# Optimization experiments

Measured on AMD Instinct MI355X. Metric: run time of the kernel, lower is better.

## Reference

```python
import jax, jax.numpy as jnp
import numpy as np
import math

EMBED_DIM = 256
NUM_HEADS = 8
FFN_DIM = 1024
EPS = 1e-5


def layer_norm(x, g, b):
    mu = jnp.mean(x, axis=-1, keepdims=True)
    var = jnp.var(x, axis=-1, keepdims=True)
    return (x - mu) / jnp.sqrt(var + EPS) * g + b


def setup_inputs() -> dict:
    key = jax.random.key(0)
    ks = jax.random.split(key, 10)
    B, L, D, F = 4, 2048, EMBED_DIM, FFN_DIM
    x = jax.random.normal(ks[0], (B, L, D), dtype=jnp.float32)
    mask = jnp.ones((B, L), dtype=jnp.int32)
    # FFN params (PyTorch Linear default-ish scale)
    W1 = jax.random.normal(ks[1], (D, F), dtype=jnp.float32) / np.sqrt(D)
    b1 = jnp.zeros((F,), dtype=jnp.float32)
    W2 = jax.random.normal(ks[2], (F, D), dtype=jnp.float32) / np.sqrt(F)
    b2 = jnp.zeros((D,), dtype=jnp.float32)
    g1 = jnp.ones((D,), dtype=jnp.float32)
    be1 = jnp.zeros((D,), dtype=jnp.float32)
    g2 = jnp.ones((D,), dtype=jnp.float32)
    be2 = jnp.zeros((D,), dtype=jnp.float32)
    return {"x": x, "mask": mask, "W1": W1, "b1": b1, "W2": W2, "b2": b2,
            "g1": g1, "be1": be1, "g2": g2, "be2": be2}


def quantum_attention(x, mask):
    B, L, D = x.shape
    H, dk = NUM_HEADS, D // NUM_HEADS
    xh = x.reshape(B, L, H, dk).transpose(0, 2, 1, 3)  # [B,H,L,dk]
    # per-token mean over batch and heads -> [L, dk]
    m = jnp.mean(xh, axis=(0, 1))
    # closed form of the single-qubit RX circuit: P(|1>) = sin^2(angle/2)
    dot = m @ m.T  # [L, L]
    ang = jnp.clip(dot, -math.pi, math.pi)
    scores = jnp.sin(ang * 0.5) ** 2  # [L, L], shared across B and H
    attn = jnp.broadcast_to(scores[None, None], (B, H, L, L))
    attn = jnp.where(mask[:, None, None, :] == 0, -1e9, attn)
    attn = jax.nn.softmax(attn, axis=-1)
    out = jnp.einsum('bhij,bhjd->bhid', attn, xh)  # values are xh itself
    return out.transpose(0, 2, 1, 3).reshape(B, L, D)


def reference(x, mask, W1, b1, W2, b2, g1, be1, g2, be2):
    attn_out = quantum_attention(x, mask)
    h = layer_norm(x + attn_out, g1, be1)
    ffn = jax.nn.relu(h @ W1 + b1) @ W2 + b2
    return layer_norm(h + ffn, g2, be2)
```

## Files before the change

kernel.cpp:

```cpp
#include <hip/hip_runtime.h>
#include <hip/hip_bf16.h>


#define B_ 4
#define L_ 2048
#define D_ 256
#define F_ 1024
#define PI_F 3.14159265358979323846f

typedef __bf16 bf16x8 __attribute__((ext_vector_type(8)));
typedef float floatx4 __attribute__((ext_vector_type(4)));

__device__ __forceinline__ unsigned short f2bf(float f) {
    unsigned int u = __float_as_uint(f);
    u = (u + 0x7FFFu + ((u >> 16) & 1u)) >> 16;
    return (unsigned short)u;
}
__device__ __forceinline__ float bf2f(unsigned short u) {
    union { unsigned int i; float f; } v; v.i = ((unsigned int)u) << 16; return v.f;
}

__device__ __forceinline__ void async_cp16(unsigned short* lds, const unsigned short* g) {
    __builtin_amdgcn_global_load_lds(
        (const __attribute__((address_space(1))) unsigned int*)g,
        (__attribute__((address_space(3))) unsigned int*)lds, 16, 0, 0);
}

__global__ __launch_bounds__(256) void k_prep(const float* __restrict__ x,
                                              const float* __restrict__ W1,
                                              const float* __restrict__ W2,
                                              const int* __restrict__ mask,
                                              unsigned short* __restrict__ mb,
                                              unsigned short* __restrict__ XmT,
                                              unsigned short* __restrict__ W1T,
                                              unsigned short* __restrict__ W2T) {
    __shared__ float tile[32][33];
    int r = blockIdx.x, t = threadIdx.x;
    if (r >= 2560) {
        if (r < 2816) {
            int idx = (r - 2560) * 256 + t;
            int l = idx >> 5, k = idx & 31;
            float s = 0.f;
#pragma unroll
            for (int b = 0; b < B_; b++) {
                const float* xp = x + ((size_t)(b * L_ + l)) * D_ + k;
#pragma unroll
                for (int h = 0; h < 8; h++) s += xp[h * 32];
            }
            mb[idx] = f2bf(s * (1.f / 32.f));
        } else {
#pragma unroll
            for (int c = 0; c < 32; c++) {
                int e = c * 256 + t;
                int b = e >> 11, j = e & (L_ - 1);
                XmT[(size_t)(1024 + b) * L_ + j] = mask[b * L_ + j] ? 0x3F80 : 0;
            }
        }
        return;
    }
    const float* in; unsigned short* outp; int R, C; const int* mrow = nullptr; size_t bo = 0;
    int bx, by;
    if (r < 2048) {
        int z = r >> 9, rem = r & 511; by = rem >> 3; bx = rem & 7;
        in = x; outp = XmT; R = L_; C = 256; bo = (size_t)z * R * C; mrow = mask + z * L_;
    } else if (r < 2304) {
        int rem = r - 2048; bx = rem & 31; by = rem >> 5;
        in = W1; outp = W1T; R = 256; C = 1024;
    } else {
        int rem = r - 2304; bx = rem & 7; by = rem >> 3;
        in = W2; outp = W2T; R = 1024; C = 256;
    }
    int r0 = by * 32, c0 = bx * 32;
    int tx = t & 31, ty = t >> 5;
#pragma unroll
    for (int rr = 0; rr < 4; rr++) {
        int rw = ty + rr * 8;
        tile[rw][tx] = in[bo + (size_t)(r0 + rw) * C + c0 + tx];
    }
    float mfac = 1.f;
    if (mrow) mfac = mrow[r0 + tx] ? 1.f : 0.f;
    __syncthreads();
#pragma unroll
    for (int rr = 0; rr < 4; rr++) {
        int c = ty + rr * 8;
        outp[bo + (size_t)(c0 + c) * R + r0 + tx] = f2bf(tile[tx][c] * mfac);
    }
}

__global__ __launch_bounds__(256) void k_scores_mfma(const unsigned short* __restrict__ mb,
                                                     unsigned short* __restrict__ E) {
    const int t = threadIdx.x, lane = t & 63, wid = t >> 6;
    const int wm = (wid >> 1) * 64, wn = (wid & 1) * 32;
    const int lr = lane & 15, lq = lane >> 4;
    int m0 = blockIdx.y * 128, n0 = blockIdx.x * 64;
    bf16x8 af[4], bfr[2];
#pragma unroll
    for (int i = 0; i < 4; i++)
        af[i] = *(const bf16x8*)(mb + (size_t)(m0 + wm + i * 16 + lr) * 32 + lq * 8);
#pragma unroll
    for (int j = 0; j < 2; j++)
        bfr[j] = *(const bf16x8*)(mb + (size_t)(n0 + wn + j * 16 + lr) * 32 + lq * 8);
    floatx4 acc[4][2];
#pragma unroll
    for (int i = 0; i < 4; i++)
#pragma unroll
        for (int j = 0; j < 2; j++) {
            acc[i][j] = (floatx4){0.f, 0.f, 0.f, 0.f};
            acc[i][j] = __builtin_amdgcn_mfma_f32_16x16x32_bf16(af[i], bfr[j], acc[i][j], 0, 0, 0);
        }
#pragma unroll
    for (int i = 0; i < 4; i++)
#pragma unroll
        for (int j = 0; j < 2; j++)
#pragma unroll
            for (int r = 0; r < 4; r++) {
                int row = m0 + wm + i * 16 + lq * 4 + r;
                int col = n0 + wn + j * 16 + lr;
                float d = fminf(fmaxf(acc[i][j][r], -PI_F), PI_F);
                float sn = __sinf(0.5f * d);
                E[(size_t)row * L_ + col] = f2bf(__expf(sn * sn));
            }
}

__device__ __forceinline__ void mfma_gemm_async(const unsigned short* __restrict__ A,
                                                const unsigned short* __restrict__ Bt,
                                                int K, int m0, int n0,
                                                unsigned short* sA, unsigned short* sB,
                                                floatx4 acc[4][2]) {
    const int t = threadIdx.x;
    const int lane = t & 63, wid = t >> 6;
    const int wm = (wid >> 1) * 64, wn = (wid & 1) * 32;
    const int lr = lane & 15, lq = lane >> 4;
    const int lrow = lane >> 3, lseg = lane & 7;

    const unsigned short* Ag[4]; unsigned short* sAd[4];
#pragma unroll
    for (int q = 0; q < 4; q++) {
        int rl = wid * 32 + q * 8 + lrow;
        int seg = (lseg - rl) & 7;
        Ag[q] = A + (size_t)(m0 + rl) * K + seg * 8;
        sAd[q] = sA + (wid * 32 + q * 8) * 64;
    }
    const unsigned short* Bg[2]; unsigned short* sBd[2];
#pragma unroll
    for (int q = 0; q < 2; q++) {
        int rl = wid * 16 + q * 8 + lrow;
        int seg = (lseg - rl) & 7;
        Bg[q] = Bt + (size_t)(n0 + rl) * K + seg * 8;
        sBd[q] = sB + (wid * 16 + q * 8) * 64;
    }
    int arot[4], brot[2];
    const unsigned short* sAr[4]; const unsigned short* sBr[2];
#pragma unroll
    for (int i = 0; i < 4; i++) { int ar = wm + i * 16 + lr; sAr[i] = sA + ar * 64; arot[i] = lq + ar; }
#pragma unroll
    for (int j = 0; j < 2; j++) { int br = wn + j * 16 + lr; sBr[j] = sB + br * 64; brot[j] = lq + br; }

    for (int k0 = 0; k0 < K; k0 += 64) {
        __syncthreads();
#pragma unroll
        for (int q = 0; q < 4; q++) async_cp16(sAd[q], Ag[q] + k0);
#pragma unroll
        for (int q = 0; q < 2; q++) async_cp16(sBd[q], Bg[q] + k0);
        __syncthreads();
#pragma unroll
        for (int s = 0; s < 2; s++) {
            bf16x8 af[4], bfr[2];
#pragma unroll
            for (int i = 0; i < 4; i++)
                af[i] = *(const bf16x8*)(sAr[i] + ((s * 4 + arot[i]) & 7) * 8);
#pragma unroll
            for (int j = 0; j < 2; j++)
                bfr[j] = *(const bf16x8*)(sBr[j] + ((s * 4 + brot[j]) & 7) * 8);
#pragma unroll
            for (int i = 0; i < 4; i++)
#pragma unroll
                for (int j = 0; j < 2; j++)
                    acc[i][j] = __builtin_amdgcn_mfma_f32_16x16x32_bf16(af[i], bfr[j], acc[i][j], 0, 0, 0);
        }
    }
}

__global__ __launch_bounds__(256) void k_av(const unsigned short* __restrict__ E,
                                            const unsigned short* __restrict__ XmT,
                                            unsigned short* __restrict__ Cb) {
    __shared__ __align__(16) unsigned short sA[128 * 64];
    __shared__ __align__(16) unsigned short sB[64 * 64];
    floatx4 acc[4][2];
#pragma unroll
    for (int i = 0; i < 4; i++)
#pragma unroll
        for (int j = 0; j < 2; j++) acc[i][j] = (floatx4){0.f, 0.f, 0.f, 0.f};
    int m0 = blockIdx.y * 128, n0 = blockIdx.x * 64;
    mfma_gemm_async(E, XmT, L_, m0, n0, sA, sB, acc);
    const int lane = threadIdx.x & 63, wid = threadIdx.x >> 6;
    const int wm = (wid >> 1) * 64, wn = (wid & 1) * 32;
    const int lr = lane & 15, lq = lane >> 4;
#pragma unroll
    for (int i = 0; i < 4; i++)
#pragma unroll
        for (int j = 0; j < 2; j++)
#pragma unroll
            for (int r = 0; r < 4; r++) {
                int row = m0 + wm + i * 16 + lq * 4 + r;
                int col = n0 + wn + j * 16 + lr;
                Cb[(size_t)row * 1088 + col] = f2bf(acc[i][j][r]);
            }
}

__global__ __launch_bounds__(256) void k_ln1(const float* __restrict__ x, const unsigned short* __restrict__ Cb,
                                             const float* __restrict__ g_, const float* __restrict__ be_,
                                             unsigned short* __restrict__ hb) {
    int tok = blockIdx.x, t = threadIdx.x;
    int b = tok >> 11, i = tok & (L_ - 1);
    float rs = bf2f(Cb[(size_t)i * 1088 + 1024 + b]);
    float v = x[(size_t)tok * D_ + t] + bf2f(Cb[(size_t)i * 1088 + b * 256 + t]) / rs;
    float s = v, s2 = v * v;
    __shared__ float sm[8];
#pragma unroll
    for (int o = 1; o < 64; o <<= 1) { s += __shfl_xor(s, o); s2 += __shfl_xor(s2, o); }
    if ((t & 63) == 0) { sm[t >> 6] = s; sm[4 + (t >> 6)] = s2; }
    __syncthreads();
    s = sm[0] + sm[1] + sm[2] + sm[3];
    s2 = sm[4] + sm[5] + sm[6] + sm[7];
    float mu = s * (1.f / 256.f);
    float var = s2 * (1.f / 256.f) - mu * mu;
    float r = rsqrtf(var + 1e-5f);
    hb[(size_t)tok * D_ + t] = f2bf((v - mu) * r * g_[t] + be_[t]);
}

__global__ __launch_bounds__(256) void k_gemm1(const unsigned short* __restrict__ hb,
                                               const unsigned short* __restrict__ W1T,
                                               const float* __restrict__ b1, unsigned short* __restrict__ t1) {
    __shared__ __align__(16) unsigned short sA[128 * 64];
    __shared__ __align__(16) unsigned short sB[128 * 64];
    const int t = threadIdx.x, lane = t & 63, wid = t >> 6;
    const int wm = (wid >> 1) * 64, wn = (wid & 1) * 64;
    const int lr = lane & 15, lq = lane >> 4;
    const int lrow8 = lane >> 3, lseg = lane & 7;
    int m0 = blockIdx.y * 128, n0 = blockIdx.x * 128;

    const unsigned short* Ag[4]; unsigned short* sAd[4];
    const unsigned short* Bg[4]; unsigned short* sBd[4];
#pragma unroll
    for (int q = 0; q < 4; q++) {
        int rl = q * 32 + wid * 8 + lrow8;
        int seg = (lseg - rl) & 7;
        Ag[q] = hb + (size_t)(m0 + rl) * 256 + seg * 8;
        Bg[q] = W1T + (size_t)(n0 + rl) * 256 + seg * 8;
        sAd[q] = sA + (q * 32 + wid * 8) * 64;
        sBd[q] = sB + (q * 32 + wid * 8) * 64;
    }
    const unsigned short* sAr[4]; int arot[4];
    const unsigned short* sBr[4]; int brot[4];
#pragma unroll
    for (int i = 0; i < 4; i++) { int ar = wm + i * 16 + lr; sAr[i] = sA + ar * 64; arot[i] = lq + ar; }
#pragma unroll
    for (int j = 0; j < 4; j++) { int br = wn + j * 16 + lr; sBr[j] = sB + br * 64; brot[j] = lq + br; }

    floatx4 acc[4][4];
#pragma unroll
    for (int i = 0; i < 4; i++)
#pragma unroll
        for (int j = 0; j < 4; j++) acc[i][j] = (floatx4){0.f, 0.f, 0.f, 0.f};

    for (int k0 = 0; k0 < 256; k0 += 64) {
        __syncthreads();
#pragma unroll
        for (int q = 0; q < 4; q++) { async_cp16(sAd[q], Ag[q] + k0); async_cp16(sBd[q], Bg[q] + k0); }
        __syncthreads();
#pragma unroll
        for (int s = 0; s < 2; s++) {
            bf16x8 af[4], bfr[4];
#pragma unroll
            for (int i = 0; i < 4; i++) af[i] = *(const bf16x8*)(sAr[i] + ((s * 4 + arot[i]) & 7) * 8);
#pragma unroll
            for (int j = 0; j < 4; j++) bfr[j] = *(const bf16x8*)(sBr[j] + ((s * 4 + brot[j]) & 7) * 8);
#pragma unroll
            for (int i = 0; i < 4; i++)
#pragma unroll
                for (int j = 0; j < 4; j++)
                    acc[i][j] = __builtin_amdgcn_mfma_f32_16x16x32_bf16(af[i], bfr[j], acc[i][j], 0, 0, 0);
        }
    }
    float bb[4];
#pragma unroll
    for (int j = 0; j < 4; j++) bb[j] = b1[n0 + wn + j * 16 + lr];
#pragma unroll
    for (int i = 0; i < 4; i++)
#pragma unroll
        for (int j = 0; j < 4; j++) {
            int col = n0 + wn + j * 16 + lr;
#pragma unroll
            for (int r = 0; r < 4; r++) {
                int row = m0 + wm + i * 16 + lq * 4 + r;
                t1[(size_t)row * 1024 + col] = f2bf(fmaxf(acc[i][j][r] + bb[j], 0.f));
            }
        }
}

__global__ __launch_bounds__(256) void k_gemm2ln(const unsigned short* __restrict__ t1,
                                                 const unsigned short* __restrict__ W2T,
                                                 const float* __restrict__ b2,
                                                 const unsigned short* __restrict__ hb,
                                                 const float* __restrict__ g_, const float* __restrict__ be_,
                                                 float* __restrict__ out) {
    __shared__ __align__(16) unsigned short sA[32 * 64];
    __shared__ __align__(16) unsigned short sB[256 * 64];
    __shared__ float red[2][32][2];
    const int t = threadIdx.x, lane = t & 63, wid = t >> 6;
    const int wm = (wid >> 1) * 16, wn = (wid & 1) * 128;
    const int lr = lane & 15, lq = lane >> 4;
    const int lrow8 = lane >> 3, lseg = lane & 7;
    int m0 = blockIdx.x * 32;

    int arl = wid * 8 + lrow8;
    const unsigned short* Ag = t1 + (size_t)(m0 + arl) * 1024 + (((lseg - arl) & 7) * 8);
    unsigned short* sAd = sA + (wid * 8) * 64;
    const unsigned short* Bg[8]; unsigned short* sBd[8];
#pragma unroll
    for (int q = 0; q < 8; q++) {
        int rl = q * 32 + wid * 8 + lrow8;
        Bg[q] = W2T + (size_t)rl * 1024 + (((lseg - rl) & 7) * 8);
        sBd[q] = sB + (q * 32 + wid * 8) * 64;
    }
    const unsigned short* sAr = sA + (wm + lr) * 64; int arot = lq + wm + lr;
    const unsigned short* sBr[8]; int brot[8];
#pragma unroll
    for (int j = 0; j < 8; j++) { int br = wn + j * 16 + lr; sBr[j] = sB + br * 64; brot[j] = lq + br; }

    floatx4 acc[8];
#pragma unroll
    for (int j = 0; j < 8; j++) acc[j] = (floatx4){0.f, 0.f, 0.f, 0.f};

    for (int k0 = 0; k0 < 1024; k0 += 64) {
        __syncthreads();
        async_cp16(sAd, Ag + k0);
#pragma unroll
        for (int q = 0; q < 8; q++) async_cp16(sBd[q], Bg[q] + k0);
        __syncthreads();
#pragma unroll
        for (int s = 0; s < 2; s++) {
            bf16x8 af = *(const bf16x8*)(sAr + ((s * 4 + arot) & 7) * 8);
#pragma unroll
            for (int j = 0; j < 8; j++) {
                bf16x8 bfr = *(const bf16x8*)(sBr[j] + ((s * 4 + brot[j]) & 7) * 8);
                acc[j] = __builtin_amdgcn_mfma_f32_16x16x32_bf16(af, bfr, acc[j], 0, 0, 0);
            }
        }
    }
    float psum[4], psq[4];
#pragma unroll
    for (int r = 0; r < 4; r++) { psum[r] = 0.f; psq[r] = 0.f; }
#pragma unroll
    for (int j = 0; j < 8; j++) {
        int col = wn + j * 16 + lr;
        float bv = b2[col];
#pragma unroll
        for (int r = 0; r < 4; r++) {
            int row = m0 + wm + lq * 4 + r;
            float v = acc[j][r] + bv + bf2f(hb[(size_t)row * 256 + col]);
            acc[j][r] = v;
            psum[r] += v; psq[r] += v * v;
        }
    }
#pragma unroll
    for (int o = 1; o < 16; o <<= 1) {
#pragma unroll
        for (int r = 0; r < 4; r++) { psum[r] += __shfl_xor(psum[r], o); psq[r] += __shfl_xor(psq[r], o); }
    }
    if (lr == 0) {
#pragma unroll
        for (int r = 0; r < 4; r++) {
            int lrow = wm + lq * 4 + r;
            red[wid & 1][lrow][0] = psum[r];
            red[wid & 1][lrow][1] = psq[r];
        }
    }
    __syncthreads();
#pragma unroll
    for (int r = 0; r < 4; r++) {
        int lrow = wm + lq * 4 + r;
        float s = red[0][lrow][0] + red[1][lrow][0];
        float s2 = red[0][lrow][1] + red[1][lrow][1];
        float mu = s * (1.f / 256.f);
        float var = s2 * (1.f / 256.f) - mu * mu;
        float rc = rsqrtf(var + 1e-5f);
        int row = m0 + lrow;
#pragma unroll
        for (int j = 0; j < 8; j++) {
            int col = wn + j * 16 + lr;
            out[(size_t)row * 256 + col] = (acc[j][r] - mu) * rc * g_[col] + be_[col];
        }
    }
}

extern "C" void kernel_launch(void* const* d_in, const int* in_sizes, int n_in,
                              void* d_out, int out_size, void* d_ws, size_t ws_size,
                              hipStream_t stream) {
    const float* x   = (const float*)d_in[0];
    const int*  mask = (const int*)d_in[1];
    const float* W1  = (const float*)d_in[2];
    const float* b1  = (const float*)d_in[3];
    const float* W2  = (const float*)d_in[4];
    const float* b2  = (const float*)d_in[5];
    const float* g1  = (const float*)d_in[6];
    const float* be1 = (const float*)d_in[7];
    const float* g2  = (const float*)d_in[8];
    const float* be2 = (const float*)d_in[9];
    float* out = (float*)d_out;

    char* w = (char*)d_ws;
    unsigned short* mb_   = (unsigned short*)w;  w += 65536 * 2;
    unsigned short* E_    = (unsigned short*)w;  w += (size_t)L_ * L_ * 2;
    unsigned short* XmT_  = (unsigned short*)w;  w += (size_t)1088 * L_ * 2;
    unsigned short* W1T_  = (unsigned short*)w;  w += 262144 * 2;
    unsigned short* W2T_  = (unsigned short*)w;  w += 262144 * 2;
    unsigned short* Cb_   = (unsigned short*)w;  w += (size_t)L_ * 1088 * 2;
    unsigned short* hb_   = (unsigned short*)w;  w += (size_t)8192 * 256 * 2;
    unsigned short* t1_   = (unsigned short*)w;  w += (size_t)8192 * 1024 * 2;

    k_prep<<<2817, 256, 0, stream>>>(x, W1, W2, mask, mb_, XmT_, W1T_, W2T_);
    k_scores_mfma<<<dim3(32, 16), 256, 0, stream>>>(mb_, E_);
    k_av<<<dim3(17, 16), 256, 0, stream>>>(E_, XmT_, Cb_);
    k_ln1<<<B_ * L_, 256, 0, stream>>>(x, Cb_, g1, be1, hb_);
    k_gemm1<<<dim3(8, 64), 256, 0, stream>>>(hb_, W1T_, b1, t1_);
    k_gemm2ln<<<256, 256, 0, stream>>>(t1_, W2T_, b2, hb_, g2, be2, out);
}
```

Baseline: 150.8 us.

## Fuse all stages into one cooperative persistent kernel with grid syncs

Turns the six separate kernel launches into a single cooperative kernel of 256 blocks. The blocks loop over each stage's work units and separate the stages with grid.sync(), which removes the per-launch overhead and the gaps between kernels. If the cooperative launch fails, the code falls back to the old sequence of wrapper kernels. In exchange, the stages are now limited to 256 resident blocks, so stages with more work (prep with 2817 units, ln1 with 8192) run many serial iterations per block. The shared memory is also sized for the largest stage, which may reduce occupancy.

```diff
diff --git a/kernel.cpp b/kernel.cpp
--- a/kernel.cpp
+++ b/kernel.cpp
@@ -1,5 +1,6 @@
 #include <hip/hip_runtime.h>
 #include <hip/hip_bf16.h>
+#include <hip/hip_cooperative_groups.h>
 
 
 #define B_ 4
@@ -8,6 +9,8 @@
 #define F_ 1024
 #define PI_F 3.14159265358979323846f
 
+namespace cg = cooperative_groups;
+
 typedef __bf16 bf16x8 __attribute__((ext_vector_type(8)));
 typedef float floatx4 __attribute__((ext_vector_type(4)));
 
@@ -26,16 +29,19 @@
         (__attribute__((address_space(3))) unsigned int*)lds, 16, 0, 0);
 }
 
-__global__ __launch_bounds__(256) void k_prep(const float* __restrict__ x,
-                                              const float* __restrict__ W1,
-                                              const float* __restrict__ W2,
-                                              const int* __restrict__ mask,
-                                              unsigned short* __restrict__ mb,
-                                              unsigned short* __restrict__ XmT,
-                                              unsigned short* __restrict__ W1T,
-                                              unsigned short* __restrict__ W2T) {
-    __shared__ float tile[32][33];
-    int r = blockIdx.x, t = threadIdx.x;
+#define SMEM_BYTES 37376
+
+__device__ __forceinline__ void prep_unit(int r, char* smem,
+                                          const float* __restrict__ x,
+                                          const float* __restrict__ W1,
+                                          const float* __restrict__ W2,
+                                          const int* __restrict__ mask,
+                                          unsigned short* __restrict__ mb,
+                                          unsigned short* __restrict__ XmT,
+                                          unsigned short* __restrict__ W1T,
+                                          unsigned short* __restrict__ W2T) {
+    float* tile = (float*)smem;
+    int t = threadIdx.x;
     if (r >= 2560) {
         if (r < 2816) {
             int idx = (r - 2560) * 256 + t;
@@ -72,10 +78,11 @@
     }
     int r0 = by * 32, c0 = bx * 32;
     int tx = t & 31, ty = t >> 5;
+    __syncthreads();
 #pragma unroll
     for (int rr = 0; rr < 4; rr++) {
         int rw = ty + rr * 8;
-        tile[rw][tx] = in[bo + (size_t)(r0 + rw) * C + c0 + tx];
+        tile[rw * 33 + tx] = in[bo + (size_t)(r0 + rw) * C + c0 + tx];
     }
     float mfac = 1.f;
     if (mrow) mfac = mrow[r0 + tx] ? 1.f : 0.f;
@@ -83,16 +90,16 @@
 #pragma unroll
     for (int rr = 0; rr < 4; rr++) {
         int c = ty + rr * 8;
-        outp[bo + (size_t)(c0 + c) * R + r0 + tx] = f2bf(tile[tx][c] * mfac);
-    }
-}
-
-__global__ __launch_bounds__(256) void k_scores_mfma(const unsigned short* __restrict__ mb,
-                                                     unsigned short* __restrict__ E) {
+        outp[bo + (size_t)(c0 + c) * R + r0 + tx] = f2bf(tile[tx * 33 + c] * mfac);
+    }
+}
+
+__device__ __forceinline__ void scores_unit(int u, const unsigned short* __restrict__ mb,
+                                            unsigned short* __restrict__ E) {
     const int t = threadIdx.x, lane = t & 63, wid = t >> 6;
     const int wm = (wid >> 1) * 64, wn = (wid & 1) * 32;
     const int lr = lane & 15, lq = lane >> 4;
-    int m0 = blockIdx.y * 128, n0 = blockIdx.x * 64;
+    int m0 = (u >> 5) * 128, n0 = (u & 31) * 64;
     bf16x8 af[4], bfr[2];
 #pragma unroll
     for (int i = 0; i < 4; i++)
@@ -181,17 +188,18 @@
     }
 }
 
-__global__ __launch_bounds__(256) void k_av(const unsigned short* __restrict__ E,
-                                            const unsigned short* __restrict__ XmT,
-                                            unsigned short* __restrict__ Cb) {
-    __shared__ __align__(16) unsigned short sA[128 * 64];
-    __shared__ __align__(16) unsigned short sB[64 * 64];
+__device__ __forceinline__ void av_unit(int u, char* smem,
+                                        const unsigned short* __restrict__ E,
+                                        const unsigned short* __restrict__ XmT,
+                                        unsigned short* __restrict__ Cb) {
+    unsigned short* sA = (unsigned short*)smem;
+    unsigned short* sB = (unsigned short*)(smem + 16384);
     floatx4 acc[4][2];
 #pragma unroll
     for (int i = 0; i < 4; i++)
 #pragma unroll
         for (int j = 0; j < 2; j++) acc[i][j] = (floatx4){0.f, 0.f, 0.f, 0.f};
-    int m0 = blockIdx.y * 128, n0 = blockIdx.x * 64;
+    int m0 = (u / 17) * 128, n0 = (u % 17) * 64;
     mfma_gemm_async(E, XmT, L_, m0, n0, sA, sB, acc);
     const int lane = threadIdx.x & 63, wid = threadIdx.x >> 6;
     const int wm = (wid >> 1) * 64, wn = (wid & 1) * 32;
@@ -208,17 +216,19 @@
             }
 }
 
-__global__ __launch_bounds__(256) void k_ln1(const float* __restrict__ x, const unsigned short* __restrict__ Cb,
-                                             const float* __restrict__ g_, const float* __restrict__ be_,
-                                             unsigned short* __restrict__ hb) {
-    int tok = blockIdx.x, t = threadIdx.x;
+__device__ __forceinline__ void ln1_unit(int tok, char* smem,
+                                         const float* __restrict__ x, const unsigned short* __restrict__ Cb,
+                                         const float* __restrict__ g_, const float* __restrict__ be_,
+                                         unsigned short* __restrict__ hb) {
+    float* sm = (float*)smem;
+    int t = threadIdx.x;
     int b = tok >> 11, i = tok & (L_ - 1);
     float rs = bf2f(Cb[(size_t)i * 1088 + 1024 + b]);
     float v = x[(size_t)tok * D_ + t] + bf2f(Cb[(size_t)i * 1088 + b * 256 + t]) / rs;
     float s = v, s2 = v * v;
-    __shared__ float sm[8];
 #pragma unroll
     for (int o = 1; o < 64; o <<= 1) { s += __shfl_xor(s, o); s2 += __shfl_xor(s2, o); }
+    __syncthreads();
     if ((t & 63) == 0) { sm[t >> 6] = s; sm[4 + (t >> 6)] = s2; }
     __syncthreads();
     s = sm[0] + sm[1] + sm[2] + sm[3];
@@ -229,16 +239,17 @@
     hb[(size_t)tok * D_ + t] = f2bf((v - mu) * r * g_[t] + be_[t]);
 }
 
-__global__ __launch_bounds__(256) void k_gemm1(const unsigned short* __restrict__ hb,
-                                               const unsigned short* __restrict__ W1T,
-                                               const float* __restrict__ b1, unsigned short* __restrict__ t1) {
-    __shared__ __align__(16) unsigned short sA[128 * 64];
-    __shared__ __align__(16) unsigned short sB[128 * 64];
+__device__ __forceinline__ void gemm1_unit(int u, char* smem,
+                                           const unsigned short* __restrict__ hb,
+                                           const unsigned short* __restrict__ W1T,
+                                           const float* __restrict__ b1, unsigned short* __restrict__ t1) {
+    unsigned short* sA = (unsigned short*)smem;
+    unsigned short* sB = (unsigned short*)(smem + 16384);
     const int t = threadIdx.x, lane = t & 63, wid = t >> 6;
     const int wm = (wid >> 1) * 64, wn = (wid & 1) * 64;
     const int lr = lane & 15, lq = lane >> 4;
     const int lrow8 = lane >> 3, lseg = lane & 7;
-    int m0 = blockIdx.y * 128, n0 = blockIdx.x * 128;
+    int m0 = (u >> 3) * 128, n0 = (u & 7) * 128;
 
     const unsigned short* Ag[4]; unsigned short* sAd[4];
     const unsigned short* Bg[4]; unsigned short* sBd[4];
@@ -299,20 +310,21 @@
         }
 }
 
-__global__ __launch_bounds__(256) void k_gemm2ln(const unsigned short* __restrict__ t1,
-                                                 const unsigned short* __restrict__ W2T,
-                                                 const float* __restrict__ b2,
-                                                 const unsigned short* __restrict__ hb,
-                                                 const float* __restrict__ g_, const float* __restrict__ be_,
-                                                 float* __restrict__ out) {
-    __shared__ __align__(16) unsigned short sA[32 * 64];
-    __shared__ __align__(16) unsigned short sB[256 * 64];
-    __shared__ float red[2][32][2];
+__device__ __forceinline__ void gemm2ln_unit(int u, char* smem,
+                                             const unsigned short* __restrict__ t1,
+                                             const unsigned short* __restrict__ W2T,
+                                             const float* __restrict__ b2,
+                                             const unsigned short* __restrict__ hb,
+                                             const float* __restrict__ g_, const float* __restrict__ be_,
+                                             float* __restrict__ out) {
+    unsigned short* sA = (unsigned short*)smem;
+    unsigned short* sB = (unsigned short*)(smem + 4096);
+    float* red = (float*)(smem + 36864);
     const int t = threadIdx.x, lane = t & 63, wid = t >> 6;
     const int wm = (wid >> 1) * 16, wn = (wid & 1) * 128;
     const int lr = lane & 15, lq = lane >> 4;
     const int lrow8 = lane >> 3, lseg = lane & 7;
-    int m0 = blockIdx.x * 32;
+    int m0 = u * 32;
 
     int arl = wid * 8 + lrow8;
     const unsigned short* Ag = t1 + (size_t)(m0 + arl) * 1024 + (((lseg - arl) & 7) * 8);
@@ -369,20 +381,21 @@
 #pragma unroll
         for (int r = 0; r < 4; r++) { psum[r] += __shfl_xor(psum[r], o); psq[r] += __shfl_xor(psq[r], o); }
     }
+    __syncthreads();
     if (lr == 0) {
 #pragma unroll
         for (int r = 0; r < 4; r++) {
             int lrow = wm + lq * 4 + r;
-            red[wid & 1][lrow][0] = psum[r];
-            red[wid & 1][lrow][1] = psq[r];
+            red[(((wid & 1) * 32) + lrow) * 2 + 0] = psum[r];
+            red[(((wid & 1) * 32) + lrow) * 2 + 1] = psq[r];
         }
     }
     __syncthreads();
 #pragma unroll
     for (int r = 0; r < 4; r++) {
         int lrow = wm + lq * 4 + r;
-        float s = red[0][lrow][0] + red[1][lrow][0];
-        float s2 = red[0][lrow][1] + red[1][lrow][1];
+        float s = red[lrow * 2 + 0] + red[(32 + lrow) * 2 + 0];
+        float s2 = red[lrow * 2 + 1] + red[(32 + lrow) * 2 + 1];
         float mu = s * (1.f / 256.f);
         float var = s2 * (1.f / 256.f) - mu * mu;
         float rc = rsqrtf(var + 1e-5f);
@@ -393,6 +406,85 @@
             out[(size_t)row * 256 + col] = (acc[j][r] - mu) * rc * g_[col] + be_[col];
         }
     }
+}
+
+__global__ __launch_bounds__(256) void k_mega(const float* __restrict__ x,
+                                              const int* __restrict__ mask,
+                                              const float* __restrict__ W1,
+                                              const float* __restrict__ b1,
+                                              const float* __restrict__ W2,
+                                              const float* __restrict__ b2,
+                                              const float* __restrict__ g1,
+                                              const float* __restrict__ be1,
+                                              const float* __restrict__ g2,
+                                              const float* __restrict__ be2,
+                                              float* __restrict__ out,
+                                              char* __restrict__ ws) {
+    __shared__ __align__(16) char smem[SMEM_BYTES];
+    cg::grid_group grid = cg::this_grid();
+    const int bid = blockIdx.x;
+
+    unsigned short* mb_  = (unsigned short*)ws;
+    unsigned short* E_   = (unsigned short*)(ws + 0x0020000);
+    unsigned short* XmT_ = (unsigned short*)(ws + 0x0820000);
+    unsigned short* W1T_ = (unsigned short*)(ws + 0x0C60000);
+    unsigned short* W2T_ = (unsigned short*)(ws + 0x0CE0000);
+    unsigned short* Cb_  = (unsigned short*)(ws + 0x0D60000);
+    unsigned short* hb_  = (unsigned short*)(ws + 0x11A0000);
+    unsigned short* t1_  = (unsigned short*)(ws + 0x15A0000);
+
+#pragma unroll 1
+    for (int u = bid; u < 2817; u += 256)
+        prep_unit(u, smem, x, W1, W2, mask, mb_, XmT_, W1T_, W2T_);
+    grid.sync();
+#pragma unroll 1
+    for (int u = bid; u < 512; u += 256)
+        scores_unit(u, mb_, E_);
+    grid.sync();
+#pragma unroll 1
+    for (int u = bid; u < 272; u += 256)
+        av_unit(u, smem, E_, XmT_, Cb_);
+    grid.sync();
+#pragma unroll 1
+    for (int it = 0; it < 32; it++)
+        ln1_unit(it * 256 + bid, smem, x, Cb_, g1, be1, hb_);
+    grid.sync();
+#pragma unroll 1
+    for (int u = bid; u < 512; u += 256)
+        gemm1_unit(u, smem, hb_, W1T_, b1, t1_);
+    grid.sync();
+    gemm2ln_unit(bid, smem, t1_, W2T_, b2, hb_, g2, be2, out);
+}
+
+__global__ __launch_bounds__(256) void k_prep_w(const float* x, const float* W1, const float* W2,
+                                                const int* mask, unsigned short* mb, unsigned short* XmT,
+                                                unsigned short* W1T, unsigned short* W2T) {
+    __shared__ __align__(16) char smem[4352];
+    prep_unit(blockIdx.x, smem, x, W1, W2, mask, mb, XmT, W1T, W2T);
+}
+__global__ __launch_bounds__(256) void k_scores_w(const unsigned short* mb, unsigned short* E) {
+    scores_unit(blockIdx.x, mb, E);
+}
+__global__ __launch_bounds__(256) void k_av_w(const unsigned short* E, const unsigned short* XmT,
+                                              unsigned short* Cb) {
+    __shared__ __align__(16) char smem[24576];
+    av_unit(blockIdx.x, smem, E, XmT, Cb);
+}
+__global__ __launch_bounds__(256) void k_ln1_w(const float* x, const unsigned short* Cb,
+                                               const float* g1, const float* be1, unsigned short* hb) {
+    __shared__ __align__(16) char smem[64];
+    ln1_unit(blockIdx.x, smem, x, Cb, g1, be1, hb);
+}
+__global__ __launch_bounds__(256) void k_gemm1_w(const unsigned short* hb, const unsigned short* W1T,
+                                                 const float* b1, unsigned short* t1) {
+    __shared__ __align__(16) char smem[32768];
+    gemm1_unit(blockIdx.x, smem, hb, W1T, b1, t1);
+}
+__global__ __launch_bounds__(256) void k_gemm2ln_w(const unsigned short* t1, const unsigned short* W2T,
+                                                   const float* b2, const unsigned short* hb,
+                                                   const float* g2, const float* be2, float* out) {
+    __shared__ __align__(16) char smem[SMEM_BYTES];
+    gemm2ln_unit(blockIdx.x, smem, t1, W2T, b2, hb, g2, be2, out);
 }
 
 extern "C" void kernel_launch(void* const* d_in, const int* in_sizes, int n_in,
@@ -409,21 +501,27 @@
     const float* g2  = (const float*)d_in[8];
     const float* be2 = (const float*)d_in[9];
     float* out = (float*)d_out;
-
-    char* w = (char*)d_ws;
-    unsigned short* mb_   = (unsigned short*)w;  w += 65536 * 2;
-    unsigned short* E_    = (unsigned short*)w;  w += (size_t)L_ * L_ * 2;
-    unsigned short* XmT_  = (unsigned short*)w;  w += (size_t)1088 * L_ * 2;
-    unsigned short* W1T_  = (unsigned short*)w;  w += 262144 * 2;
-    unsigned short* W2T_  = (unsigned short*)w;  w += 262144 * 2;
-    unsigned short* Cb_   = (unsigned short*)w;  w += (size_t)L_ * 1088 * 2;
-    unsigned short* hb_   = (unsigned short*)w;  w += (size_t)8192 * 256 * 2;
-    unsigned short* t1_   = (unsigned short*)w;  w += (size_t)8192 * 1024 * 2;
-
-    k_prep<<<2817, 256, 0, stream>>>(x, W1, W2, mask, mb_, XmT_, W1T_, W2T_);
-    k_scores_mfma<<<dim3(32, 16), 256, 0, stream>>>(mb_, E_);
-    k_av<<<dim3(17, 16), 256, 0, stream>>>(E_, XmT_, Cb_);
-    k_ln1<<<B_ * L_, 256, 0, stream>>>(x, Cb_, g1, be1, hb_);
-    k_gemm1<<<dim3(8, 64), 256, 0, stream>>>(hb_, W1T_, b1, t1_);
-    k_gemm2ln<<<256, 256, 0, stream>>>(t1_, W2T_, b2, hb_, g2, be2, out);
-}
+    char* ws = (char*)d_ws;
+
+    unsigned short* mb_  = (unsigned short*)ws;
+    unsigned short* E_   = (unsigned short*)(ws + 0x0020000);
+    unsigned short* XmT_ = (unsigned short*)(ws + 0x0820000);
+    unsigned short* W1T_ = (unsigned short*)(ws + 0x0C60000);
+    unsigned short* W2T_ = (unsigned short*)(ws + 0x0CE0000);
+    unsigned short* Cb_  = (unsigned short*)(ws + 0x0D60000);
+    unsigned short* hb_  = (unsigned short*)(ws + 0x11A0000);
+    unsigned short* t1_  = (unsigned short*)(ws + 0x15A0000);
+
+    void* args[] = {(void*)&x, (void*)&mask, (void*)&W1, (void*)&b1, (void*)&W2, (void*)&b2,
+                    (void*)&g1, (void*)&be1, (void*)&g2, (void*)&be2, (void*)&out, (void*)&ws};
+    hipError_t e = hipLaunchCooperativeKernel((const void*)k_mega, dim3(256), dim3(256), args, 0, stream);
+    if (e != hipSuccess) {
+        (void)hipGetLastError();
+        k_prep_w<<<2817, 256, 0, stream>>>(x, W1, W2, mask, mb_, XmT_, W1T_, W2T_);
+        k_scores_w<<<512, 256, 0, stream>>>(mb_, E_);
+        k_av_w<<<272, 256, 0, stream>>>(E_, XmT_, Cb_);
+        k_ln1_w<<<8192, 256, 0, stream>>>(x, Cb_, g1, be1, hb_);
+        k_gemm1_w<<<512, 256, 0, stream>>>(hb_, W1T_, b1, t1_);
+        k_gemm2ln_w<<<256, 256, 0, stream>>>(t1_, W2T_, b2, hb_, g2, be2, out);
+    }
+}
```

Measured after the change: 370.3 us. +145.5%, slower.
